# Optimization experiments

Hardware: AMD Instinct MI355X
Metric: run time of the kernel (lower is better)

## Reference

```python
import jax, jax.numpy as jnp
import numpy as np

N = 100000
E = 1600000
IN = 128
H = 256
K = 7          # n_hops + 1
INTERVAL = 3
R = K - INTERVAL + 1  # n_relations + 1 = 5


def setup_inputs() -> dict:
    key = jax.random.key(0)
    ks = jax.random.split(key, 8)
    features = jax.random.normal(ks[0], (N, IN), dtype=jnp.float32)
    W1 = jax.random.normal(ks[1], (K, IN, H), dtype=jnp.float32) * (1.0 / np.sqrt(IN))
    b1 = jnp.zeros((K, H), dtype=jnp.float32)
    W2 = jax.random.normal(ks[2], (K, H, H), dtype=jnp.float32) * (1.0 / np.sqrt(H))
    b2 = jnp.zeros((K, H), dtype=jnp.float32)
    Wr = jax.random.normal(ks[3], (R, H * INTERVAL, H), dtype=jnp.float32) * (1.0 / np.sqrt(H * INTERVAL))
    br = jnp.zeros((R, H), dtype=jnp.float32)
    row = jax.random.randint(ks[4], (E,), 0, N, dtype=jnp.int64)
    col = jax.random.randint(ks[5], (E,), 0, N, dtype=jnp.int64)
    return {"features": features, "W1": W1, "b1": b1, "W2": W2, "b2": b2,
            "Wr": Wr, "br": br, "row": row, "col": col}


def _norm_adj(row, col):
    # set_diag=True: add self loops; symm_norm: D^-1/2 (A+I) D^-1/2
    diag = jnp.arange(N, dtype=row.dtype)
    r = jnp.concatenate([row, diag])
    c = jnp.concatenate([col, diag])
    deg = jax.ops.segment_sum(jnp.ones_like(r, dtype=jnp.float32), r, num_segments=N)
    dinv = jnp.where(deg > 0, jax.lax.rsqrt(deg), 0.0)
    w = dinv[r] * dinv[c]  # [E+N]
    return r, c, w


def _forward(features, W1, b1, W2, b2, Wr, br, row, col):
    r, c, w = _norm_adj(row, col)

    def spmm(x):  # x: [N, F] -> A_hat @ x
        return jax.ops.segment_sum(x[c] * w[:, None], r, num_segments=N)

    def step(x, _):
        nx = spmm(x)
        return nx, nx

    _, hops = jax.lax.scan(step, features, None, length=K - 1)  # [K-1, N, IN]
    hop_feats = jnp.concatenate([features[None], hops], axis=0)  # [K, N, IN]

    # per-hop DeepSets (2-layer MLP with ReLU): [K, N, H]
    h = jax.nn.relu(jnp.einsum('kni,kih->knh', hop_feats, W1) + b1[:, None, :])
    h = jnp.einsum('knh,khg->kng', h, W2) + b2[:, None, :]

    hops_feats = jnp.transpose(h, (1, 0, 2))  # [N, K, H]
    # sliding windows of INTERVAL hops: [R, N, INTERVAL*H]
    wins = jnp.stack([hops_feats[:, i:i + INTERVAL, :].reshape(N, INTERVAL * H)
                      for i in range(R)], axis=0)
    rel = jax.nn.relu(jnp.einsum('rnd,rdh->rnh', wins, Wr) + br[:, None, :])  # [R, N, H]
    out = jnp.transpose(rel, (1, 0, 2)).reshape(N, R * H)  # concat over relations
    return out


def reference(features, W1, b1, W2, b2, Wr, br, row, col):
    return _forward(features, W1, b1, W2, b2, Wr, br, row, col)
```

## Files before the change

kernel.cpp:

```cpp
#include <hip/hip_runtime.h>

#define N_NODES 100000
#define E_EDGES 1600000
#define IN_F 128
#define H_F 256
#define K_HOPS 7
#define R_REL 5
#define OUT_W (R_REL * H_F)
#define SCAN_B ((N_NODES + 1023) / 1024)

typedef __attribute__((ext_vector_type(8))) short short8;
typedef __attribute__((ext_vector_type(4))) float f32x4;

#define GLOAD16(g, l) __builtin_amdgcn_global_load_lds( \
    (const __attribute__((address_space(1))) void*)(g), \
    (__attribute__((address_space(3))) void*)(l), 16, 0, 0)


__global__ void zero_int(int* __restrict__ p, int n) {
    int t = blockIdx.x * blockDim.x + threadIdx.x;
    if (t < n) p[t] = 0;
}

__global__ void deg_count(const int* __restrict__ row, int* __restrict__ deg) {
    int e = blockIdx.x * blockDim.x + threadIdx.x;
    if (e < E_EDGES) atomicAdd(&deg[row[e]], 1);
}

__global__ void dinv_compute(const int* __restrict__ deg, float* __restrict__ dinv) {
    int i = blockIdx.x * blockDim.x + threadIdx.x;
    if (i < N_NODES) dinv[i] = rsqrtf((float)(deg[i] + 1));
}

__global__ __launch_bounds__(1024) void scan1(const int* __restrict__ deg,
                                              int* __restrict__ rp, int* __restrict__ bsum) {
    __shared__ int ws[16];
    const int t = threadIdx.x, lane = t & 63, wv = t >> 6;
    int i = blockIdx.x * 1024 + t;
    int v = (i < N_NODES) ? deg[i] : 0;
    int x = v;
#pragma unroll
    for (int off = 1; off < 64; off <<= 1) {
        int n = __shfl_up(x, off, 64);
        if (lane >= off) x += n;
    }
    if (lane == 63) ws[wv] = x;
    __syncthreads();
    if (wv == 0 && lane < 16) {
        int s = ws[lane];
#pragma unroll
        for (int off = 1; off < 16; off <<= 1) {
            int n = __shfl_up(s, off, 64);
            if (lane >= off) s += n;
        }
        ws[lane] = s;
    }
    __syncthreads();
    int wbase = (wv == 0) ? 0 : ws[wv - 1];
    if (i < N_NODES) rp[i] = wbase + x - v;
    if (t == 1023) bsum[blockIdx.x] = ws[15];
}

__global__ __launch_bounds__(128) void scan2(int* __restrict__ bsum) {
    __shared__ int wtot[2];
    const int t = threadIdx.x, lane = t & 63, wv = t >> 6;
    int v = (t < SCAN_B) ? bsum[t] : 0;
    int x = v;
#pragma unroll
    for (int off = 1; off < 64; off <<= 1) {
        int n = __shfl_up(x, off, 64);
        if (lane >= off) x += n;
    }
    if (lane == 63) wtot[wv] = x;
    __syncthreads();
    int base = (wv == 1) ? wtot[0] : 0;
    if (t < SCAN_B) bsum[t] = base + x - v;
    if (t == 127) bsum[SCAN_B] = wtot[0] + wtot[1];
}

__global__ __launch_bounds__(1024) void scan3(int* __restrict__ rp,
                                              const int* __restrict__ bsum) {
    int i = blockIdx.x * 1024 + threadIdx.x;
    if (i < N_NODES) rp[i] += bsum[blockIdx.x];
    if (i == 0) rp[N_NODES] = bsum[SCAN_B];
}

__global__ void csr_scatter(const int* __restrict__ row, const int* __restrict__ col,
                            const float* __restrict__ dinv, const int* __restrict__ rowptr,
                            int* __restrict__ cursor, int* __restrict__ cols2,
                            float* __restrict__ ew) {
    int e = blockIdx.x * blockDim.x + threadIdx.x;
    if (e >= E_EDGES) return;
    int r = row[e], c = col[e];
    int pos = rowptr[r] + atomicAdd(&cursor[r], 1);
    cols2[pos] = c;
    ew[pos] = dinv[r] * dinv[c];
}

__global__ __launch_bounds__(256) void spmm_csr(
    const float4* __restrict__ x, const int* __restrict__ rowptr,
    const int* __restrict__ cols, const float* __restrict__ w,
    const float* __restrict__ dinv, float4* __restrict__ y) {
    const int wave = threadIdx.x >> 6, lane = threadIdx.x & 63;
    const int i = blockIdx.x * 4 + wave;
    if (i >= N_NODES) return;
    const int fh = lane & 31;
    const int slot = lane >> 5;
    const int jb = rowptr[i];
    const int cnt = rowptr[i + 1] - jb;

    float4 acc = make_float4(0.f, 0.f, 0.f, 0.f);
    int t = slot;
    for (; t + 6 < cnt; t += 8) {
        int c0 = cols[jb + t],     c1 = cols[jb + t + 2];
        int c2 = cols[jb + t + 4], c3 = cols[jb + t + 6];
        float ww0 = w[jb + t],     ww1 = w[jb + t + 2];
        float ww2 = w[jb + t + 4], ww3 = w[jb + t + 6];
        float4 v0 = x[(size_t)c0 * 32 + fh];
        float4 v1 = x[(size_t)c1 * 32 + fh];
        float4 v2 = x[(size_t)c2 * 32 + fh];
        float4 v3 = x[(size_t)c3 * 32 + fh];
        acc.x += ww0 * v0.x + ww1 * v1.x + ww2 * v2.x + ww3 * v3.x;
        acc.y += ww0 * v0.y + ww1 * v1.y + ww2 * v2.y + ww3 * v3.y;
        acc.z += ww0 * v0.z + ww1 * v1.z + ww2 * v2.z + ww3 * v3.z;
        acc.w += ww0 * v0.w + ww1 * v1.w + ww2 * v2.w + ww3 * v3.w;
    }
    for (; t < cnt; t += 2) {
        int c0 = cols[jb + t];
        float ww0 = w[jb + t];
        float4 v0 = x[(size_t)c0 * 32 + fh];
        acc.x += ww0 * v0.x;
        acc.y += ww0 * v0.y;
        acc.z += ww0 * v0.z;
        acc.w += ww0 * v0.w;
    }
    acc.x += __shfl_xor(acc.x, 32);
    acc.y += __shfl_xor(acc.y, 32);
    acc.z += __shfl_xor(acc.z, 32);
    acc.w += __shfl_xor(acc.w, 32);
    if (slot == 0) {
        float d = dinv[i];
        float s = d * d;
        float4 xv = x[(size_t)i * 32 + fh];
        acc.x += s * xv.x;
        acc.y += s * xv.y;
        acc.z += s * xv.z;
        acc.w += s * xv.w;
        y[(size_t)i * 32 + fh] = acc;
    }
}


__device__ __forceinline__ void f2bf_split(float v, short& h, short& l) {
    unsigned u = __float_as_uint(v);
    unsigned hb = (u + 0x7FFFu + ((u >> 16) & 1u)) >> 16;
    float fh = __uint_as_float(hb << 16);
    float r = v - fh;
    unsigned u2 = __float_as_uint(r);
    unsigned lb = (u2 + 0x7FFFu + ((u2 >> 16) & 1u)) >> 16;
    h = (short)(unsigned short)hb;
    l = (short)(unsigned short)lb;
}

__global__ __launch_bounds__(256) void wc_compute(const float* __restrict__ W2,
                                                  const float* __restrict__ Wr,
                                                  float* __restrict__ Wc) {
    __shared__ float as[8][256];
    const int z = blockIdx.x, j0 = blockIdx.y * 8, g = threadIdx.x;
    const int r = z / 3, d = z % 3, hop = r + d;
    const float* a = W2 + (size_t)hop * H_F * H_F + (size_t)j0 * H_F;
    for (int t = threadIdx.x; t < 8 * 256; t += 256)
        as[t >> 8][t & 255] = a[t];
    __syncthreads();
    const float* b = Wr + ((size_t)r * 768 + (size_t)d * H_F) * H_F + g;
    float acc[8] = {0.f, 0.f, 0.f, 0.f, 0.f, 0.f, 0.f, 0.f};
    for (int h = 0; h < H_F; ++h) {
        float bv = b[(size_t)h * H_F];
#pragma unroll
        for (int jj = 0; jj < 8; ++jj) acc[jj] += as[jj][h] * bv;
    }
#pragma unroll
    for (int jj = 0; jj < 8; ++jj)
        Wc[(size_t)z * H_F * H_F + (size_t)(j0 + jj) * H_F + g] = acc[jj];
}

__global__ __launch_bounds__(256) void bc_compute(const float* __restrict__ b2,
                                                  const float* __restrict__ Wr,
                                                  const float* __restrict__ br,
                                                  float* __restrict__ bc) {
    const int r = blockIdx.x, g = threadIdx.x;
    float acc = br[(size_t)r * H_F + g];
    for (int t = 0; t < 3 * H_F; ++t) {
        float bv = b2[(size_t)(r + t / H_F) * H_F + (t % H_F)];
        acc += bv * Wr[((size_t)r * 768 + t) * H_F + g];
    }
    bc[(size_t)r * H_F + g] = acc;
}

__global__ void transpose_convert(const float* __restrict__ in, short* __restrict__ oh,
                                  short* __restrict__ ol, int Kd, int grp) {
    __shared__ float t[32][33];
    const int i0 = blockIdx.x * 32, n0 = blockIdx.y * 32, z = blockIdx.z;
    const int tx = threadIdx.x, ty = threadIdx.y;
    const int outLd = grp * Kd;
    const float* ip = in + (size_t)z * Kd * 256;
#pragma unroll
    for (int j = 0; j < 4; ++j)
        t[ty + 8 * j][tx] = ip[(size_t)(i0 + ty + 8 * j) * 256 + n0 + tx];
    __syncthreads();
    size_t base = (size_t)(z / grp) * 256 * outLd + (size_t)(z % grp) * Kd;
#pragma unroll
    for (int j = 0; j < 4; ++j) {
        float v = t[tx][ty + 8 * j];
        short hb, lb;
        f2bf_split(v, hb, lb);
        size_t o = base + (size_t)(n0 + ty + 8 * j) * outLd + i0 + tx;
        oh[o] = hb;
        ol[o] = lb;
    }
}


#define LROW 40

__global__ __launch_bounds__(256, 2) void gemm_mlp(
    const float* __restrict__ A,
    const short* __restrict__ BTh, const short* __restrict__ BTl,
    short* __restrict__ Ch, short* __restrict__ Cl,
    const float* __restrict__ bias, int M)
{
    __shared__ short lds_buf[4 * 128 * LROW];
    short* Ah = lds_buf;
    short* Al = lds_buf + 128 * LROW;
    short* Bh = lds_buf + 2 * 128 * LROW;
    short* Bl = lds_buf + 3 * 128 * LROW;

    const int tid = threadIdx.x;
    const int lane = tid & 63, wave = tid >> 6;
    const int wm = wave & 1, wn = wave >> 1;
    const int fr = lane & 15, fg = lane >> 4;
    const int m0 = blockIdx.y * 128;
    const int n0 = blockIdx.x * 128;

    const int sr = tid >> 1;
    const int sc = (tid & 1) * 16;
    const bool avalid = (m0 + sr) < M;
    const int arow = avalid ? (m0 + sr) : (M - 1);

    f32x4 ga[4];
    short8 gbh[2], gbl[2];
    {
        const float* ap = A + (size_t)arow * IN_F + sc;
        const short* bph = BTh + (size_t)(n0 + sr) * IN_F + sc;
        const short* bpl = BTl + (size_t)(n0 + sr) * IN_F + sc;
#pragma unroll
        for (int l = 0; l < 4; ++l) ga[l] = *(const f32x4*)(ap + 4 * l);
        gbh[0] = *(const short8*)bph;  gbh[1] = *(const short8*)(bph + 8);
        gbl[0] = *(const short8*)bpl;  gbl[1] = *(const short8*)(bpl + 8);
    }

    f32x4 acc[4][4];
#pragma unroll
    for (int i = 0; i < 4; ++i)
#pragma unroll
        for (int j = 0; j < 4; ++j) acc[i][j] = (f32x4)0.f;

    const int nk = IN_F / 32;
    for (int kk = 0; kk < nk; ++kk) {
        __syncthreads();
        {
            short8 vh[2], vl[2];
#pragma unroll
            for (int l = 0; l < 4; ++l) {
                f32x4 v = ga[l];
                if (!avalid) v = (f32x4)0.f;
#pragma unroll
                for (int e = 0; e < 4; ++e) {
                    short hb, lb;
                    f2bf_split(v[e], hb, lb);
                    vh[l >> 1][(l & 1) * 4 + e] = hb;
                    vl[l >> 1][(l & 1) * 4 + e] = lb;
                }
            }
            *(short8*)(Ah + sr * LROW + sc)     = vh[0];
            *(short8*)(Ah + sr * LROW + sc + 8) = vh[1];
            *(short8*)(Al + sr * LROW + sc)     = vl[0];
            *(short8*)(Al + sr * LROW + sc + 8) = vl[1];
            *(short8*)(Bh + sr * LROW + sc)     = gbh[0];
            *(short8*)(Bh + sr * LROW + sc + 8) = gbh[1];
            *(short8*)(Bl + sr * LROW + sc)     = gbl[0];
            *(short8*)(Bl + sr * LROW + sc + 8) = gbl[1];
        }
        __syncthreads();

        if (kk + 1 < nk) {
            int k0 = (kk + 1) * 32;
            const float* ap = A + (size_t)arow * IN_F + k0 + sc;
            const short* bph = BTh + (size_t)(n0 + sr) * IN_F + k0 + sc;
            const short* bpl = BTl + (size_t)(n0 + sr) * IN_F + k0 + sc;
#pragma unroll
            for (int l = 0; l < 4; ++l) ga[l] = *(const f32x4*)(ap + 4 * l);
            gbh[0] = *(const short8*)(bph);  gbh[1] = *(const short8*)(bph + 8);
            gbl[0] = *(const short8*)(bpl);  gbl[1] = *(const short8*)(bpl + 8);
        }

        short8 afh[4], afl[4], bfh[4], bfl[4];
#pragma unroll
        for (int mf = 0; mf < 4; ++mf) {
            int r = wm * 64 + mf * 16 + fr;
            afh[mf] = *(const short8*)(Ah + r * LROW + fg * 8);
            afl[mf] = *(const short8*)(Al + r * LROW + fg * 8);
        }
#pragma unroll
        for (int nf = 0; nf < 4; ++nf) {
            int r = wn * 64 + nf * 16 + fr;
            bfh[nf] = *(const short8*)(Bh + r * LROW + fg * 8);
            bfl[nf] = *(const short8*)(Bl + r * LROW + fg * 8);
        }
#pragma unroll
        for (int mf = 0; mf < 4; ++mf)
#pragma unroll
            for (int nf = 0; nf < 4; ++nf) {
                acc[mf][nf] = __builtin_amdgcn_mfma_f32_16x16x32_bf16(
                    afh[mf], bfh[nf], acc[mf][nf], 0, 0, 0);
                acc[mf][nf] = __builtin_amdgcn_mfma_f32_16x16x32_bf16(
                    afh[mf], bfl[nf], acc[mf][nf], 0, 0, 0);
                acc[mf][nf] = __builtin_amdgcn_mfma_f32_16x16x32_bf16(
                    afl[mf], bfh[nf], acc[mf][nf], 0, 0, 0);
            }
    }

#pragma unroll
    for (int nf = 0; nf < 4; ++nf) {
        int colg = n0 + wn * 64 + nf * 16 + fr;
        float bv = bias[colg];
#pragma unroll
        for (int mf = 0; mf < 4; ++mf) {
            int rowbase = m0 + wm * 64 + mf * 16 + fg * 4;
#pragma unroll
            for (int j = 0; j < 4; ++j) {
                int rowg = rowbase + j;
                if (rowg < M) {
                    float v = fmaxf(acc[mf][nf][j] + bv, 0.f);
                    short hb, lb;
                    f2bf_split(v, hb, lb);
                    size_t idx = (size_t)rowg * H_F + colg;
                    Ch[idx] = hb;
                    Cl[idx] = lb;
                }
            }
        }
    }
}


__global__ __launch_bounds__(512, 2) void gemm_rel(
    const short* __restrict__ h1h, const short* __restrict__ h1l, long hopStride,
    const short* __restrict__ wch, const short* __restrict__ wcl,
    float* __restrict__ outB, const float* __restrict__ bcB, int M, int nwg)
{
    __shared__ short lds[2][4][8192];

    const int bid = blockIdx.x;
    const int q8 = nwg >> 3, r8 = nwg & 7;
    const int xcd = bid & 7, idx = bid >> 3;
    const int wgid = (xcd < r8) ? (xcd * (q8 + 1) + idx)
                                : (r8 * (q8 + 1) + (xcd - r8) * q8 + idx);
    const int rrel = wgid % R_REL;
    const int mblk = wgid / R_REL;
    const int m0 = mblk * 256;

    const int tid = threadIdx.x;
    const int lane = tid & 63, wave = tid >> 6;
    const int wm = wave & 1, wn = wave >> 1;
    const int fr = lane & 15, fg = lane >> 4;

    const short* Agh = h1h + (size_t)rrel * hopStride;
    const short* Agl = h1l + (size_t)rrel * hopStride;
    const short* BTh = wch + (size_t)rrel * 256 * 768;
    const short* BTl = wcl + (size_t)rrel * 256 * 768;
    float* C = outB + (size_t)rrel * H_F;
    const float* bias = bcB + (size_t)rrel * H_F;

    const int kstart = ((3 - (rrel % 3)) % 3) * 8;

    int aoff[2], boff[2], loff[2];
#pragma unroll
    for (int p = 0; p < 2; ++p) {
        int c = wave * 2 + p;
        int r = c * 16 + (lane >> 2);
        int u = lane & 3;
        int g = (u - (r >> 1)) & 3;
        int ar = m0 + r; if (ar >= M) ar = M - 1;
        aoff[p] = ar * H_F + g * 8;
        boff[p] = r * 768 + g * 8;
        loff[p] = c * 512;
    }

#define STAGE_REL(buf, kg) do {                                                  \
        int hop_ = (kg) >> 8, kin_ = (kg) & 255;                                 \
        const short* ah_ = Agh + (size_t)hop_ * hopStride + kin_;                \
        const short* al_ = Agl + (size_t)hop_ * hopStride + kin_;                \
        const short* bh_ = BTh + (kg);                                           \
        const short* bl_ = BTl + (kg);                                           \
        GLOAD16(ah_ + aoff[0], &lds[buf][0][loff[0]]);                           \
        GLOAD16(ah_ + aoff[1], &lds[buf][0][loff[1]]);                           \
        GLOAD16(al_ + aoff[0], &lds[buf][1][loff[0]]);                           \
        GLOAD16(al_ + aoff[1], &lds[buf][1][loff[1]]);                           \
        GLOAD16(bh_ + boff[0], &lds[buf][2][loff[0]]);                           \
        GLOAD16(bh_ + boff[1], &lds[buf][2][loff[1]]);                           \
        GLOAD16(bl_ + boff[0], &lds[buf][3][loff[0]]);                           \
        GLOAD16(bl_ + boff[1], &lds[buf][3][loff[1]]);                           \
    } while (0)

#define KIDX(t) ((((t) + kstart) % nk) * 32)

    f32x4 acc[8][4];
#pragma unroll
    for (int i = 0; i < 8; ++i)
#pragma unroll
        for (int j = 0; j < 4; ++j) acc[i][j] = (f32x4)0.f;

    const int nk = 768 / 32;

    STAGE_REL(0, KIDX(0));
    STAGE_REL(1, KIDX(1));

    int cur = 0;
    for (int kt = 0; kt < nk; ++kt) {
        if (kt + 1 < nk) {
            asm volatile("s_waitcnt vmcnt(8)" ::: "memory");
        } else {
            asm volatile("s_waitcnt vmcnt(0)" ::: "memory");
        }
        __builtin_amdgcn_sched_barrier(0);
        __builtin_amdgcn_s_barrier();
        __builtin_amdgcn_sched_barrier(0);

        const short* Ahc = &lds[cur][0][0];
        const short* Alc = &lds[cur][1][0];
        const short* Bhc = &lds[cur][2][0];
        const short* Blc = &lds[cur][3][0];

        short8 bfh[4], bfl[4];
#pragma unroll
        for (int nf = 0; nf < 4; ++nf) {
            int rb = wn * 64 + nf * 16 + fr;
            int ub = (fg + (rb >> 1)) & 3;
            bfh[nf] = *(const short8*)(Bhc + rb * 32 + ub * 8);
            bfl[nf] = *(const short8*)(Blc + rb * 32 + ub * 8);
        }
        __builtin_amdgcn_s_setprio(1);
#pragma unroll
        for (int mf = 0; mf < 8; ++mf) {
            int ra = wm * 128 + mf * 16 + fr;
            int ua = (fg + (ra >> 1)) & 3;
            short8 ah = *(const short8*)(Ahc + ra * 32 + ua * 8);
            short8 al = *(const short8*)(Alc + ra * 32 + ua * 8);
#pragma unroll
            for (int nf = 0; nf < 4; ++nf) {
                acc[mf][nf] = __builtin_amdgcn_mfma_f32_16x16x32_bf16(
                    ah, bfh[nf], acc[mf][nf], 0, 0, 0);
                acc[mf][nf] = __builtin_amdgcn_mfma_f32_16x16x32_bf16(
                    ah, bfl[nf], acc[mf][nf], 0, 0, 0);
                acc[mf][nf] = __builtin_amdgcn_mfma_f32_16x16x32_bf16(
                    al, bfh[nf], acc[mf][nf], 0, 0, 0);
            }
        }
        __builtin_amdgcn_s_setprio(0);

        __builtin_amdgcn_sched_barrier(0);
        __builtin_amdgcn_s_barrier();
        __builtin_amdgcn_sched_barrier(0);

        if (kt + 2 < nk) STAGE_REL(cur, KIDX(kt + 2));
        cur ^= 1;
    }

#pragma unroll
    for (int nf = 0; nf < 4; ++nf) {
        int colg = wn * 64 + nf * 16 + fr;
        float bv = bias[colg];
#pragma unroll
        for (int mf = 0; mf < 8; ++mf) {
            int rowbase = m0 + wm * 128 + mf * 16 + fg * 4;
#pragma unroll
            for (int j = 0; j < 4; ++j) {
                int rowg = rowbase + j;
                if (rowg < M)
                    C[(size_t)rowg * OUT_W + colg] = fmaxf(acc[mf][nf][j] + bv, 0.f);
            }
        }
    }
#undef STAGE_REL
#undef KIDX
}


template <int MODE>
__global__ __launch_bounds__(256, 2) void gemm_presplit(
    const short* __restrict__ Agh, const short* __restrict__ Agl, int lda,
    const short* __restrict__ BTh, const short* __restrict__ BTl, int ldb, int Kd,
    float* __restrict__ C, int ldc, const float* __restrict__ bias, int M)
{
    __shared__ short lds_buf[4 * 128 * LROW];
    short* Ah = lds_buf;
    short* Al = lds_buf + 128 * LROW;
    short* Bh = lds_buf + 2 * 128 * LROW;
    short* Bl = lds_buf + 3 * 128 * LROW;

    const int tid = threadIdx.x;
    const int lane = tid & 63, wave = tid >> 6;
    const int wm = wave & 1, wn = wave >> 1;
    const int fr = lane & 15, fg = lane >> 4;
    const int m0 = blockIdx.y * 128;
    const int n0 = blockIdx.x * 128;

    const int sr = tid >> 1;
    const int sc = (tid & 1) * 16;
    const bool avalid = (m0 + sr) < M;
    const int arow = avalid ? (m0 + sr) : (M - 1);

    short8 gah[2], gal[2], gbh[2], gbl[2];
    {
        const short* aph = Agh + (size_t)arow * lda + sc;
        const short* apl = Agl + (size_t)arow * lda + sc;
        const short* bph = BTh + (size_t)(n0 + sr) * ldb + sc;
        const short* bpl = BTl + (size_t)(n0 + sr) * ldb + sc;
        gah[0] = *(const short8*)aph;  gah[1] = *(const short8*)(aph + 8);
        gal[0] = *(const short8*)apl;  gal[1] = *(const short8*)(apl + 8);
        gbh[0] = *(const short8*)bph;  gbh[1] = *(const short8*)(bph + 8);
        gbl[0] = *(const short8*)bpl;  gbl[1] = *(const short8*)(bpl + 8);
    }

    f32x4 acc[4][4];
#pragma unroll
    for (int i = 0; i < 4; ++i)
#pragma unroll
        for (int j = 0; j < 4; ++j) acc[i][j] = (f32x4)0.f;

    const int nk = Kd / 32;
    for (int kk = 0; kk < nk; ++kk) {
        __syncthreads();
        *(short8*)(Ah + sr * LROW + sc)     = gah[0];
        *(short8*)(Ah + sr * LROW + sc + 8) = gah[1];
        *(short8*)(Al + sr * LROW + sc)     = gal[0];
        *(short8*)(Al + sr * LROW + sc + 8) = gal[1];
        *(short8*)(Bh + sr * LROW + sc)     = gbh[0];
        *(short8*)(Bh + sr * LROW + sc + 8) = gbh[1];
        *(short8*)(Bl + sr * LROW + sc)     = gbl[0];
        *(short8*)(Bl + sr * LROW + sc + 8) = gbl[1];
        __syncthreads();

        if (kk + 1 < nk) {
            int k0 = (kk + 1) * 32;
            const short* aph = Agh + (size_t)arow * lda + k0 + sc;
            const short* apl = Agl + (size_t)arow * lda + k0 + sc;
            const short* bph = BTh + (size_t)(n0 + sr) * ldb + k0 + sc;
            const short* bpl = BTl + (size_t)(n0 + sr) * ldb + k0 + sc;
            gah[0] = *(const short8*)aph;  gah[1] = *(const short8*)(aph + 8);
            gal[0] = *(const short8*)apl;  gal[1] = *(const short8*)(apl + 8);
            gbh[0] = *(const short8*)bph;  gbh[1] = *(const short8*)(bph + 8);
            gbl[0] = *(const short8*)bpl;  gbl[1] = *(const short8*)(bpl + 8);
        }

        short8 afh[4], afl[4], bfh[4], bfl[4];
#pragma unroll
        for (int mf = 0; mf < 4; ++mf) {
            int r = wm * 64 + mf * 16 + fr;
            afh[mf] = *(const short8*)(Ah + r * LROW + fg * 8);
            afl[mf] = *(const short8*)(Al + r * LROW + fg * 8);
        }
#pragma unroll
        for (int nf = 0; nf < 4; ++nf) {
            int r = wn * 64 + nf * 16 + fr;
            bfh[nf] = *(const short8*)(Bh + r * LROW + fg * 8);
            bfl[nf] = *(const short8*)(Bl + r * LROW + fg * 8);
        }
#pragma unroll
        for (int mf = 0; mf < 4; ++mf)
#pragma unroll
            for (int nf = 0; nf < 4; ++nf) {
                acc[mf][nf] = __builtin_amdgcn_mfma_f32_16x16x32_bf16(
                    afh[mf], bfh[nf], acc[mf][nf], 0, 0, 0);
                acc[mf][nf] = __builtin_amdgcn_mfma_f32_16x16x32_bf16(
                    afh[mf], bfl[nf], acc[mf][nf], 0, 0, 0);
                acc[mf][nf] = __builtin_amdgcn_mfma_f32_16x16x32_bf16(
                    afl[mf], bfh[nf], acc[mf][nf], 0, 0, 0);
            }
    }

#pragma unroll
    for (int nf = 0; nf < 4; ++nf) {
        int colg = n0 + wn * 64 + nf * 16 + fr;
        float bv = (MODE == 0) ? bias[colg] : 0.f;
#pragma unroll
        for (int mf = 0; mf < 4; ++mf) {
            int rowbase = m0 + wm * 64 + mf * 16 + fg * 4;
#pragma unroll
            for (int j = 0; j < 4; ++j) {
                int rowg = rowbase + j;
                if (rowg < M) {
                    size_t idx = (size_t)rowg * ldc + colg;
                    float v = acc[mf][nf][j] + bv;
                    if (MODE >= 2) v += C[idx];
                    if (MODE & 1) v = fmaxf(v, 0.f);
                    C[idx] = v;
                }
            }
        }
    }
}


extern "C" void kernel_launch(void* const* d_in, const int* in_sizes, int n_in,
                              void* d_out, int out_size, void* d_ws, size_t ws_size,
                              hipStream_t stream) {
    const float* features = (const float*)d_in[0];
    const float* W1 = (const float*)d_in[1];
    const float* b1 = (const float*)d_in[2];
    const float* W2 = (const float*)d_in[3];
    const float* b2 = (const float*)d_in[4];
    const float* Wr = (const float*)d_in[5];
    const float* br = (const float*)d_in[6];
    const int* row = (const int*)d_in[7];
    const int* col = (const int*)d_in[8];
    float* out = (float*)d_out;

    char* ws = (char*)d_ws;
    int* deg = (int*)ws;
    int* rowptr = (int*)(ws + (1ull << 20));
    float* dinv = (float*)(ws + (2ull << 20));
    int* bsum = (int*)(ws + (3ull << 20));
    int* cols2 = (int*)(ws + (4ull << 20));
    float* ew = (float*)(ws + (11ull << 20));
    short* w1h = (short*)(ws + (18ull << 20));
    short* w1l = (short*)(ws + (19ull << 20));
    float* wc32 = (float*)(ws + (20ull << 20));
    short* wch = (short*)(ws + (24ull << 20));
    short* wcl = (short*)(ws + (26ull << 20));
    float* bc = (float*)(ws + (28ull << 20));
    float* xa = (float*)(ws + (32ull << 20));
    float* xb = (float*)(ws + (96ull << 20));
    short* h1h = (short*)(ws + (160ull << 20));
    short* h1l = (short*)(ws + (576ull << 20));

    const bool windowed = ws_size >= (1000ull << 20);

    zero_int<<<(N_NODES + 255) / 256, 256, 0, stream>>>(deg, N_NODES);
    deg_count<<<(E_EDGES + 255) / 256, 256, 0, stream>>>(row, deg);
    dinv_compute<<<(N_NODES + 255) / 256, 256, 0, stream>>>(deg, dinv);
    scan1<<<SCAN_B, 1024, 0, stream>>>(deg, rowptr, bsum);
    scan2<<<1, 128, 0, stream>>>(bsum);
    scan3<<<SCAN_B, 1024, 0, stream>>>(rowptr, bsum);
    zero_int<<<(N_NODES + 255) / 256, 256, 0, stream>>>(deg, N_NODES);
    csr_scatter<<<(E_EDGES + 255) / 256, 256, 0, stream>>>(row, col, dinv, rowptr,
                                                           deg, cols2, ew);

    wc_compute<<<dim3(15, 32), 256, 0, stream>>>(W2, Wr, wc32);
    bc_compute<<<R_REL, 256, 0, stream>>>(b2, Wr, br, bc);

    dim3 tb(32, 8);
    transpose_convert<<<dim3(IN_F / 32, 8, K_HOPS), tb, 0, stream>>>(W1, w1h, w1l, IN_F, 1);
    transpose_convert<<<dim3(H_F / 32, 8, 15), tb, 0, stream>>>(wc32, wch, wcl, H_F, 3);

    const float* xcur = features;
    float* bufs[2] = {xa, xb};
    for (int k = 0; k < K_HOPS; ++k) {
        short* h1hd = windowed ? (h1h + (size_t)k * N_NODES * H_F) : h1h;
        short* h1ld = windowed ? (h1l + (size_t)k * N_NODES * H_F) : h1l;
        dim3 grid(2, (N_NODES + 127) / 128);
        gemm_mlp<<<grid, 256, 0, stream>>>(xcur, w1h + (size_t)k * 256 * IN_F,
                                           w1l + (size_t)k * 256 * IN_F,
                                           h1hd, h1ld, b1 + (size_t)k * H_F, N_NODES);

        if (!windowed) {
            int rlo = (k - 2 < 0) ? 0 : (k - 2);
            int rhi = (k < R_REL - 1) ? k : (R_REL - 1);
            for (int r = rlo; r <= rhi; ++r) {
                int d = k - r;
                const short* Bh = wch + (size_t)r * 256 * 768 + (size_t)d * H_F;
                const short* Bl = wcl + (size_t)r * 256 * 768 + (size_t)d * H_F;
                float* Cp = out + (size_t)r * H_F;
                if (k == r)
                    gemm_presplit<0><<<grid, 256, 0, stream>>>(
                        h1h, h1l, H_F, Bh, Bl, 768, H_F, Cp, OUT_W,
                        bc + (size_t)r * H_F, N_NODES);
                else if (k == r + 2)
                    gemm_presplit<3><<<grid, 256, 0, stream>>>(
                        h1h, h1l, H_F, Bh, Bl, 768, H_F, Cp, OUT_W, nullptr, N_NODES);
                else
                    gemm_presplit<2><<<grid, 256, 0, stream>>>(
                        h1h, h1l, H_F, Bh, Bl, 768, H_F, Cp, OUT_W, nullptr, N_NODES);
            }
        }

        if (k < K_HOPS - 1) {
            float* xn = bufs[k & 1];
            spmm_csr<<<(N_NODES + 3) / 4, 256, 0, stream>>>(
                (const float4*)xcur, rowptr, cols2, ew, dinv, (float4*)xn);
            xcur = xn;
        }
    }

    if (windowed) {
        int mblocks = (N_NODES + 255) / 256;
        int nwg = mblocks * R_REL;
        gemm_rel<<<nwg, 512, 0, stream>>>(h1h, h1l, (long)N_NODES * H_F,
                                          wch, wcl, out, bc, N_NODES, nwg);
    }
}
```

Before: 2.173 ms.

## Fuse per-hop MLP GEMM and SpMM into one interleaved launch

Adds a combined kernel in which one of every sixteen blocks runs the first-layer MLP GEMM tile for the current hop and the remaining blocks run SpMM rows that produce the next hop's features. Both parts read the same input features and have no dependency on each other, so the compute-bound GEMM and the memory-bound gather can overlap on the GPU. This also removes one launch per hop in the windowed path. In exchange, both workloads share one launch-bounds setting and one shared-memory allocation, which can limit occupancy for the SpMM blocks, and correctness depends on the block-index mapping being right.

```diff
diff --git a/kernel.cpp b/kernel.cpp
--- a/kernel.cpp
+++ b/kernel.cpp
@@ -97,13 +97,216 @@
     ew[pos] = dinv[r] * dinv[c];
 }
 
-__global__ __launch_bounds__(256) void spmm_csr(
+
+__device__ __forceinline__ void f2bf_split(float v, short& h, short& l) {
+    unsigned u = __float_as_uint(v);
+    unsigned hb = (u + 0x7FFFu + ((u >> 16) & 1u)) >> 16;
+    float fh = __uint_as_float(hb << 16);
+    float r = v - fh;
+    unsigned u2 = __float_as_uint(r);
+    unsigned lb = (u2 + 0x7FFFu + ((u2 >> 16) & 1u)) >> 16;
+    h = (short)(unsigned short)hb;
+    l = (short)(unsigned short)lb;
+}
+
+__global__ __launch_bounds__(256) void wc_compute(const float* __restrict__ W2,
+                                                  const float* __restrict__ Wr,
+                                                  float* __restrict__ Wc) {
+    __shared__ float as[8][256];
+    const int z = blockIdx.x, j0 = blockIdx.y * 8, g = threadIdx.x;
+    const int r = z / 3, d = z % 3, hop = r + d;
+    const float* a = W2 + (size_t)hop * H_F * H_F + (size_t)j0 * H_F;
+    for (int t = threadIdx.x; t < 8 * 256; t += 256)
+        as[t >> 8][t & 255] = a[t];
+    __syncthreads();
+    const float* b = Wr + ((size_t)r * 768 + (size_t)d * H_F) * H_F + g;
+    float acc[8] = {0.f, 0.f, 0.f, 0.f, 0.f, 0.f, 0.f, 0.f};
+    for (int h = 0; h < H_F; ++h) {
+        float bv = b[(size_t)h * H_F];
+#pragma unroll
+        for (int jj = 0; jj < 8; ++jj) acc[jj] += as[jj][h] * bv;
+    }
+#pragma unroll
+    for (int jj = 0; jj < 8; ++jj)
+        Wc[(size_t)z * H_F * H_F + (size_t)(j0 + jj) * H_F + g] = acc[jj];
+}
+
+__global__ __launch_bounds__(256) void bc_compute(const float* __restrict__ b2,
+                                                  const float* __restrict__ Wr,
+                                                  const float* __restrict__ br,
+                                                  float* __restrict__ bc) {
+    const int r = blockIdx.x, g = threadIdx.x;
+    float acc = br[(size_t)r * H_F + g];
+    for (int t = 0; t < 3 * H_F; ++t) {
+        float bv = b2[(size_t)(r + t / H_F) * H_F + (t % H_F)];
+        acc += bv * Wr[((size_t)r * 768 + t) * H_F + g];
+    }
+    bc[(size_t)r * H_F + g] = acc;
+}
+
+__global__ void transpose_convert(const float* __restrict__ in, short* __restrict__ oh,
+                                  short* __restrict__ ol, int Kd, int grp) {
+    __shared__ float t[32][33];
+    const int i0 = blockIdx.x * 32, n0 = blockIdx.y * 32, z = blockIdx.z;
+    const int tx = threadIdx.x, ty = threadIdx.y;
+    const int outLd = grp * Kd;
+    const float* ip = in + (size_t)z * Kd * 256;
+#pragma unroll
+    for (int j = 0; j < 4; ++j)
+        t[ty + 8 * j][tx] = ip[(size_t)(i0 + ty + 8 * j) * 256 + n0 + tx];
+    __syncthreads();
+    size_t base = (size_t)(z / grp) * 256 * outLd + (size_t)(z % grp) * Kd;
+#pragma unroll
+    for (int j = 0; j < 4; ++j) {
+        float v = t[tx][ty + 8 * j];
+        short hb, lb;
+        f2bf_split(v, hb, lb);
+        size_t o = base + (size_t)(n0 + ty + 8 * j) * outLd + i0 + tx;
+        oh[o] = hb;
+        ol[o] = lb;
+    }
+}
+
+
+#define LROW 40
+
+__device__ __forceinline__ void mlp1_body(
+    short* lds_buf, int midx,
+    const float* __restrict__ A,
+    const short* __restrict__ BTh, const short* __restrict__ BTl,
+    short* __restrict__ Ch, short* __restrict__ Cl,
+    const float* __restrict__ bias, int M)
+{
+    short* Ah = lds_buf;
+    short* Al = lds_buf + 128 * LROW;
+    short* Bh = lds_buf + 2 * 128 * LROW;
+    short* Bl = lds_buf + 3 * 128 * LROW;
+
+    const int tid = threadIdx.x;
+    const int lane = tid & 63, wave = tid >> 6;
+    const int wm = wave & 1, wn = wave >> 1;
+    const int fr = lane & 15, fg = lane >> 4;
+    const int m0 = (midx >> 1) * 128;
+    const int n0 = (midx & 1) * 128;
+
+    const int sr = tid >> 1;
+    const int sc = (tid & 1) * 16;
+    const bool avalid = (m0 + sr) < M;
+    const int arow = avalid ? (m0 + sr) : (M - 1);
+
+    f32x4 ga[4];
+    short8 gbh[2], gbl[2];
+    {
+        const float* ap = A + (size_t)arow * IN_F + sc;
+        const short* bph = BTh + (size_t)(n0 + sr) * IN_F + sc;
+        const short* bpl = BTl + (size_t)(n0 + sr) * IN_F + sc;
+#pragma unroll
+        for (int l = 0; l < 4; ++l) ga[l] = *(const f32x4*)(ap + 4 * l);
+        gbh[0] = *(const short8*)bph;  gbh[1] = *(const short8*)(bph + 8);
+        gbl[0] = *(const short8*)bpl;  gbl[1] = *(const short8*)(bpl + 8);
+    }
+
+    f32x4 acc[4][4];
+#pragma unroll
+    for (int i = 0; i < 4; ++i)
+#pragma unroll
+        for (int j = 0; j < 4; ++j) acc[i][j] = (f32x4)0.f;
+
+    const int nk = IN_F / 32;
+    for (int kk = 0; kk < nk; ++kk) {
+        __syncthreads();
+        {
+            short8 vh[2], vl[2];
+#pragma unroll
+            for (int l = 0; l < 4; ++l) {
+                f32x4 v = ga[l];
+                if (!avalid) v = (f32x4)0.f;
+#pragma unroll
+                for (int e = 0; e < 4; ++e) {
+                    short hb, lb;
+                    f2bf_split(v[e], hb, lb);
+                    vh[l >> 1][(l & 1) * 4 + e] = hb;
+                    vl[l >> 1][(l & 1) * 4 + e] = lb;
+                }
+            }
+            *(short8*)(Ah + sr * LROW + sc)     = vh[0];
+            *(short8*)(Ah + sr * LROW + sc + 8) = vh[1];
+            *(short8*)(Al + sr * LROW + sc)     = vl[0];
+            *(short8*)(Al + sr * LROW + sc + 8) = vl[1];
+            *(short8*)(Bh + sr * LROW + sc)     = gbh[0];
+            *(short8*)(Bh + sr * LROW + sc + 8) = gbh[1];
+            *(short8*)(Bl + sr * LROW + sc)     = gbl[0];
+            *(short8*)(Bl + sr * LROW + sc + 8) = gbl[1];
+        }
+        __syncthreads();
+
+        if (kk + 1 < nk) {
+            int k0 = (kk + 1) * 32;
+            const float* ap = A + (size_t)arow * IN_F + k0 + sc;
+            const short* bph = BTh + (size_t)(n0 + sr) * IN_F + k0 + sc;
+            const short* bpl = BTl + (size_t)(n0 + sr) * IN_F + k0 + sc;
+#pragma unroll
+            for (int l = 0; l < 4; ++l) ga[l] = *(const f32x4*)(ap + 4 * l);
+            gbh[0] = *(const short8*)(bph);  gbh[1] = *(const short8*)(bph + 8);
+            gbl[0] = *(const short8*)(bpl);  gbl[1] = *(const short8*)(bpl + 8);
+        }
+
+        short8 afh[4], afl[4], bfh[4], bfl[4];
+#pragma unroll
+        for (int mf = 0; mf < 4; ++mf) {
+            int r = wm * 64 + mf * 16 + fr;
+            afh[mf] = *(const short8*)(Ah + r * LROW + fg * 8);
+            afl[mf] = *(const short8*)(Al + r * LROW + fg * 8);
+        }
+#pragma unroll
+        for (int nf = 0; nf < 4; ++nf) {
+            int r = wn * 64 + nf * 16 + fr;
+            bfh[nf] = *(const short8*)(Bh + r * LROW + fg * 8);
+            bfl[nf] = *(const short8*)(Bl + r * LROW + fg * 8);
+        }
+#pragma unroll
+        for (int mf = 0; mf < 4; ++mf)
+#pragma unroll
+            for (int nf = 0; nf < 4; ++nf) {
+                acc[mf][nf] = __builtin_amdgcn_mfma_f32_16x16x32_bf16(
+                    afh[mf], bfh[nf], acc[mf][nf], 0, 0, 0);
+                acc[mf][nf] = __builtin_amdgcn_mfma_f32_16x16x32_bf16(
+                    afh[mf], bfl[nf], acc[mf][nf], 0, 0, 0);
+                acc[mf][nf] = __builtin_amdgcn_mfma_f32_16x16x32_bf16(
+                    afl[mf], bfh[nf], acc[mf][nf], 0, 0, 0);
+            }
+    }
+
+#pragma unroll
+    for (int nf = 0; nf < 4; ++nf) {
+        int colg = n0 + wn * 64 + nf * 16 + fr;
+        float bv = bias[colg];
+#pragma unroll
+        for (int mf = 0; mf < 4; ++mf) {
+            int rowbase = m0 + wm * 64 + mf * 16 + fg * 4;
+#pragma unroll
+            for (int j = 0; j < 4; ++j) {
+                int rowg = rowbase + j;
+                if (rowg < M) {
+                    float v = fmaxf(acc[mf][nf][j] + bv, 0.f);
+                    short hb, lb;
+                    f2bf_split(v, hb, lb);
+                    size_t idx = (size_t)rowg * H_F + colg;
+                    Ch[idx] = hb;
+                    Cl[idx] = lb;
+                }
+            }
+        }
+    }
+}
+
+__device__ __forceinline__ void spmm_body(
+    int i,
     const float4* __restrict__ x, const int* __restrict__ rowptr,
     const int* __restrict__ cols, const float* __restrict__ w,
-    const float* __restrict__ dinv, float4* __restrict__ y) {
-    const int wave = threadIdx.x >> 6, lane = threadIdx.x & 63;
-    const int i = blockIdx.x * 4 + wave;
-    if (i >= N_NODES) return;
+    const float* __restrict__ dinv, float4* __restrict__ y)
+{
+    const int lane = threadIdx.x & 63;
     const int fh = lane & 31;
     const int slot = lane >> 5;
     const int jb = rowptr[i];
@@ -151,78 +354,6 @@
 }
 
 
-__device__ __forceinline__ void f2bf_split(float v, short& h, short& l) {
-    unsigned u = __float_as_uint(v);
-    unsigned hb = (u + 0x7FFFu + ((u >> 16) & 1u)) >> 16;
-    float fh = __uint_as_float(hb << 16);
-    float r = v - fh;
-    unsigned u2 = __float_as_uint(r);
-    unsigned lb = (u2 + 0x7FFFu + ((u2 >> 16) & 1u)) >> 16;
-    h = (short)(unsigned short)hb;
-    l = (short)(unsigned short)lb;
-}
-
-__global__ __launch_bounds__(256) void wc_compute(const float* __restrict__ W2,
-                                                  const float* __restrict__ Wr,
-                                                  float* __restrict__ Wc) {
-    __shared__ float as[8][256];
-    const int z = blockIdx.x, j0 = blockIdx.y * 8, g = threadIdx.x;
-    const int r = z / 3, d = z % 3, hop = r + d;
-    const float* a = W2 + (size_t)hop * H_F * H_F + (size_t)j0 * H_F;
-    for (int t = threadIdx.x; t < 8 * 256; t += 256)
-        as[t >> 8][t & 255] = a[t];
-    __syncthreads();
-    const float* b = Wr + ((size_t)r * 768 + (size_t)d * H_F) * H_F + g;
-    float acc[8] = {0.f, 0.f, 0.f, 0.f, 0.f, 0.f, 0.f, 0.f};
-    for (int h = 0; h < H_F; ++h) {
-        float bv = b[(size_t)h * H_F];
-#pragma unroll
-        for (int jj = 0; jj < 8; ++jj) acc[jj] += as[jj][h] * bv;
-    }
-#pragma unroll
-    for (int jj = 0; jj < 8; ++jj)
-        Wc[(size_t)z * H_F * H_F + (size_t)(j0 + jj) * H_F + g] = acc[jj];
-}
-
-__global__ __launch_bounds__(256) void bc_compute(const float* __restrict__ b2,
-                                                  const float* __restrict__ Wr,
-                                                  const float* __restrict__ br,
-                                                  float* __restrict__ bc) {
-    const int r = blockIdx.x, g = threadIdx.x;
-    float acc = br[(size_t)r * H_F + g];
-    for (int t = 0; t < 3 * H_F; ++t) {
-        float bv = b2[(size_t)(r + t / H_F) * H_F + (t % H_F)];
-        acc += bv * Wr[((size_t)r * 768 + t) * H_F + g];
-    }
-    bc[(size_t)r * H_F + g] = acc;
-}
-
-__global__ void transpose_convert(const float* __restrict__ in, short* __restrict__ oh,
-                                  short* __restrict__ ol, int Kd, int grp) {
-    __shared__ float t[32][33];
-    const int i0 = blockIdx.x * 32, n0 = blockIdx.y * 32, z = blockIdx.z;
-    const int tx = threadIdx.x, ty = threadIdx.y;
-    const int outLd = grp * Kd;
-    const float* ip = in + (size_t)z * Kd * 256;
-#pragma unroll
-    for (int j = 0; j < 4; ++j)
-        t[ty + 8 * j][tx] = ip[(size_t)(i0 + ty + 8 * j) * 256 + n0 + tx];
-    __syncthreads();
-    size_t base = (size_t)(z / grp) * 256 * outLd + (size_t)(z % grp) * Kd;
-#pragma unroll
-    for (int j = 0; j < 4; ++j) {
-        float v = t[tx][ty + 8 * j];
-        short hb, lb;
-        f2bf_split(v, hb, lb);
-        size_t o = base + (size_t)(n0 + ty + 8 * j) * outLd + i0 + tx;
-        oh[o] = hb;
-        ol[o] = lb;
-    }
-}
-
-
-#define LROW 40
-
 __global__ __launch_bounds__(256, 2) void gemm_mlp(
     const float* __restrict__ A,
     const short* __restrict__ BTh, const short* __restrict__ BTl,
@@ -230,126 +361,37 @@
     const float* __restrict__ bias, int M)
 {
     __shared__ short lds_buf[4 * 128 * LROW];
-    short* Ah = lds_buf;
-    short* Al = lds_buf + 128 * LROW;
-    short* Bh = lds_buf + 2 * 128 * LROW;
-    short* Bl = lds_buf + 3 * 128 * LROW;
-
-    const int tid = threadIdx.x;
-    const int lane = tid & 63, wave = tid >> 6;
-    const int wm = wave & 1, wn = wave >> 1;
-    const int fr = lane & 15, fg = lane >> 4;
-    const int m0 = blockIdx.y * 128;
-    const int n0 = blockIdx.x * 128;
-
-    const int sr = tid >> 1;
-    const int sc = (tid & 1) * 16;
-    const bool avalid = (m0 + sr) < M;
-    const int arow = avalid ? (m0 + sr) : (M - 1);
-
-    f32x4 ga[4];
-    short8 gbh[2], gbl[2];
-    {
-        const float* ap = A + (size_t)arow * IN_F + sc;
-        const short* bph = BTh + (size_t)(n0 + sr) * IN_F + sc;
-        const short* bpl = BTl + (size_t)(n0 + sr) * IN_F + sc;
-#pragma unroll
-        for (int l = 0; l < 4; ++l) ga[l] = *(const f32x4*)(ap + 4 * l);
-        gbh[0] = *(const short8*)bph;  gbh[1] = *(const short8*)(bph + 8);
-        gbl[0] = *(const short8*)bpl;  gbl[1] = *(const short8*)(bpl + 8);
-    }
-
-    f32x4 acc[4][4];
-#pragma unroll
-    for (int i = 0; i < 4; ++i)
-#pragma unroll
-        for (int j = 0; j < 4; ++j) acc[i][j] = (f32x4)0.f;
-
-    const int nk = IN_F / 32;
-    for (int kk = 0; kk < nk; ++kk) {
-        __syncthreads();
-        {
-            short8 vh[2], vl[2];
-#pragma unroll
-            for (int l = 0; l < 4; ++l) {
-                f32x4 v = ga[l];
-                if (!avalid) v = (f32x4)0.f;
-#pragma unroll
-                for (int e = 0; e < 4; ++e) {
-                    short hb, lb;
-                    f2bf_split(v[e], hb, lb);
-                    vh[l >> 1][(l & 1) * 4 + e] = hb;
-                    vl[l >> 1][(l & 1) * 4 + e] = lb;
-                }
-            }
-            *(short8*)(Ah + sr * LROW + sc)     = vh[0];
-            *(short8*)(Ah + sr * LROW + sc + 8) = vh[1];
-            *(short8*)(Al + sr * LROW + sc)     = vl[0];
-            *(short8*)(Al + sr * LROW + sc + 8) = vl[1];
-            *(short8*)(Bh + sr * LROW + sc)     = gbh[0];
-            *(short8*)(Bh + sr * LROW + sc + 8) = gbh[1];
-            *(short8*)(Bl + sr * LROW + sc)     = gbl[0];
-            *(short8*)(Bl + sr * LROW + sc + 8) = gbl[1];
-        }
-        __syncthreads();
-
-        if (kk + 1 < nk) {
-            int k0 = (kk + 1) * 32;
-            const float* ap = A + (size_t)arow * IN_F + k0 + sc;
-            const short* bph = BTh + (size_t)(n0 + sr) * IN_F + k0 + sc;
-            const short* bpl = BTl + (size_t)(n0 + sr) * IN_F + k0 + sc;
-#pragma unroll
-            for (int l = 0; l < 4; ++l) ga[l] = *(const f32x4*)(ap + 4 * l);
-            gbh[0] = *(const short8*)(bph);  gbh[1] = *(const short8*)(bph + 8);
-            gbl[0] = *(const short8*)(bpl);  gbl[1] = *(const short8*)(bpl + 8);
-        }
-
-        short8 afh[4], afl[4], bfh[4], bfl[4];
-#pragma unroll
-        for (int mf = 0; mf < 4; ++mf) {
-            int r = wm * 64 + mf * 16 + fr;
-            afh[mf] = *(const short8*)(Ah + r * LROW + fg * 8);
-            afl[mf] = *(const short8*)(Al + r * LROW + fg * 8);
-        }
-#pragma unroll
-        for (int nf = 0; nf < 4; ++nf) {
-            int r = wn * 64 + nf * 16 + fr;
-            bfh[nf] = *(const short8*)(Bh + r * LROW + fg * 8);
-            bfl[nf] = *(const short8*)(Bl + r * LROW + fg * 8);
-        }
-#pragma unroll
-        for (int mf = 0; mf < 4; ++mf)
-#pragma unroll
-            for (int nf = 0; nf < 4; ++nf) {
-                acc[mf][nf] = __builtin_amdgcn_mfma_f32_16x16x32_bf16(
-                    afh[mf], bfh[nf], acc[mf][nf], 0, 0, 0);
-                acc[mf][nf] = __builtin_amdgcn_mfma_f32_16x16x32_bf16(
-                    afh[mf], bfl[nf], acc[mf][nf], 0, 0, 0);
-                acc[mf][nf] = __builtin_amdgcn_mfma_f32_16x16x32_bf16(
-                    afl[mf], bfh[nf], acc[mf][nf], 0, 0, 0);
-            }
-    }
-
-#pragma unroll
-    for (int nf = 0; nf < 4; ++nf) {
-        int colg = n0 + wn * 64 + nf * 16 + fr;
-        float bv = bias[colg];
-#pragma unroll
-        for (int mf = 0; mf < 4; ++mf) {
-            int rowbase = m0 + wm * 64 + mf * 16 + fg * 4;
-#pragma unroll
-            for (int j = 0; j < 4; ++j) {
-                int rowg = rowbase + j;
-                if (rowg < M) {
-                    float v = fmaxf(acc[mf][nf][j] + bv, 0.f);
-                    short hb, lb;
-                    f2bf_split(v, hb, lb);
-                    size_t idx = (size_t)rowg * H_F + colg;
-                    Ch[idx] = hb;
-                    Cl[idx] = lb;
-                }
-            }
-        }
+    mlp1_body(lds_buf, blockIdx.x, A, BTh, BTl, Ch, Cl, bias, M);
+}
+
+__global__ __launch_bounds__(256) void spmm_csr(
+    const float4* __restrict__ x, const int* __restrict__ rowptr,
+    const int* __restrict__ cols, const float* __restrict__ w,
+    const float* __restrict__ dinv, float4* __restrict__ y) {
+    const int i = blockIdx.x * 4 + (threadIdx.x >> 6);
+    if (i < N_NODES) spmm_body(i, x, rowptr, cols, w, dinv, y);
+}
+
+
+__global__ __launch_bounds__(256, 4) void mlp_spmm(
+    const float* __restrict__ xcur,
+    const short* __restrict__ BTh, const short* __restrict__ BTl,
+    short* __restrict__ Ch, short* __restrict__ Cl,
+    const float* __restrict__ bias,
+    const int* __restrict__ rowptr, const int* __restrict__ cols,
+    const float* __restrict__ w, const float* __restrict__ dinv,
+    float4* __restrict__ y, int nm)
+{
+    __shared__ short lds_buf[4 * 128 * LROW];
+    const int bid = blockIdx.x;
+    const int thresh = nm * 16;
+    if (bid < thresh && (bid & 15) == 0) {
+        mlp1_body(lds_buf, bid >> 4, xcur, BTh, BTl, Ch, Cl, bias, N_NODES);
+    } else {
+        int sidx = (bid < thresh) ? (bid - (bid >> 4) - 1) : (bid - nm);
+        int i = sidx * 4 + (threadIdx.x >> 6);
+        if (i < N_NODES)
+            spmm_body(i, (const float4*)xcur, rowptr, cols, w, dinv, y);
     }
 }
 
@@ -666,40 +708,51 @@
 
     const float* xcur = features;
     float* bufs[2] = {xa, xb};
+    const int nm = 2 * ((N_NODES + 127) / 128);
+    const int ns = (N_NODES + 3) / 4;
     for (int k = 0; k < K_HOPS; ++k) {
         short* h1hd = windowed ? (h1h + (size_t)k * N_NODES * H_F) : h1h;
         short* h1ld = windowed ? (h1l + (size_t)k * N_NODES * H_F) : h1l;
-        dim3 grid(2, (N_NODES + 127) / 128);
-        gemm_mlp<<<grid, 256, 0, stream>>>(xcur, w1h + (size_t)k * 256 * IN_F,
-                                           w1l + (size_t)k * 256 * IN_F,
-                                           h1hd, h1ld, b1 + (size_t)k * H_F, N_NODES);
-
-        if (!windowed) {
-            int rlo = (k - 2 < 0) ? 0 : (k - 2);
-            int rhi = (k < R_REL - 1) ? k : (R_REL - 1);
-            for (int r = rlo; r <= rhi; ++r) {
-                int d = k - r;
-                const short* Bh = wch + (size_t)r * 256 * 768 + (size_t)d * H_F;
-                const short* Bl = wcl + (size_t)r * 256 * 768 + (size_t)d * H_F;
-                float* Cp = out + (size_t)r * H_F;
-                if (k == r)
-                    gemm_presplit<0><<<grid, 256, 0, stream>>>(
-                        h1h, h1l, H_F, Bh, Bl, 768, H_F, Cp, OUT_W,
-                        bc + (size_t)r * H_F, N_NODES);
-                else if (k == r + 2)
-                    gemm_presplit<3><<<grid, 256, 0, stream>>>(
-                        h1h, h1l, H_F, Bh, Bl, 768, H_F, Cp, OUT_W, nullptr, N_NODES);
-                else
-                    gemm_presplit<2><<<grid, 256, 0, stream>>>(
-                        h1h, h1l, H_F, Bh, Bl, 768, H_F, Cp, OUT_W, nullptr, N_NODES);
+
+        if (windowed && k < K_HOPS - 1) {
+            float* xn = bufs[k & 1];
+            mlp_spmm<<<nm + ns, 256, 0, stream>>>(
+                xcur, w1h + (size_t)k * 256 * IN_F, w1l + (size_t)k * 256 * IN_F,
+                h1hd, h1ld, b1 + (size_t)k * H_F,
+                rowptr, cols2, ew, dinv, (float4*)xn, nm);
+            xcur = xn;
+        } else {
+            dim3 grid(2, (N_NODES + 127) / 128);
+            gemm_mlp<<<dim3(nm), 256, 0, stream>>>(
+                xcur, w1h + (size_t)k * 256 * IN_F, w1l + (size_t)k * 256 * IN_F,
+                h1hd, h1ld, b1 + (size_t)k * H_F, N_NODES);
+
+            if (!windowed) {
+                int rlo = (k - 2 < 0) ? 0 : (k - 2);
+                int rhi = (k < R_REL - 1) ? k : (R_REL - 1);
+                for (int r = rlo; r <= rhi; ++r) {
+                    int d = k - r;
+                    const short* Bh = wch + (size_t)r * 256 * 768 + (size_t)d * H_F;
+                    const short* Bl = wcl + (size_t)r * 256 * 768 + (size_t)d * H_F;
+                    float* Cp = out + (size_t)r * H_F;
+                    if (k == r)
+                        gemm_presplit<0><<<grid, 256, 0, stream>>>(
+                            h1h, h1l, H_F, Bh, Bl, 768, H_F, Cp, OUT_W,
+                            bc + (size_t)r * H_F, N_NODES);
+                    else if (k == r + 2)
+                        gemm_presplit<3><<<grid, 256, 0, stream>>>(
+                            h1h, h1l, H_F, Bh, Bl, 768, H_F, Cp, OUT_W, nullptr, N_NODES);
+                    else
+                        gemm_presplit<2><<<grid, 256, 0, stream>>>(
+                            h1h, h1l, H_F, Bh, Bl, 768, H_F, Cp, OUT_W, nullptr, N_NODES);
+                }
+                if (k < K_HOPS - 1) {
+                    float* xn = bufs[k & 1];
+                    spmm_csr<<<ns, 256, 0, stream>>>(
+                        (const float4*)xcur, rowptr, cols2, ew, dinv, (float4*)xn);
+                    xcur = xn;
+                }
             }
-        }
-
-        if (k < K_HOPS - 1) {
-            float* xn = bufs[k & 1];
-            spmm_csr<<<(N_NODES + 3) / 4, 256, 0, stream>>>(
-                (const float4*)xcur, rowptr, cols2, ew, dinv, (float4*)xn);
-            xcur = xn;
         }
     }
 
```

Result: slower. 4.589 ms (+111.2%).

## Interleave next-tile global-to-LDS prefetch with MFMA phases in relation GEMM

Applied to the files above, without the earlier changes.

The relation GEMM's k-loop is split into four MFMA phases, each covering two row fragments. The next k-tile's global_load_lds copies are spread across the phase boundaries, so each LDS chunk is refilled as soon as every wave has consumed it, instead of issuing all prefetches after the full compute block. The goal is to overlap memory traffic with MFMA work and hide the load latency. In exchange there are four barrier pairs per iteration instead of one, plus an lgkmcnt(0) wait in every phase, which adds synchronisation overhead.

```diff
diff --git a/kernel.cpp b/kernel.cpp
--- a/kernel.cpp
+++ b/kernel.cpp
@@ -354,6 +354,44 @@
 }
 
 
+__device__ __forceinline__ f32x4 mfma16(short8 a, short8 b, f32x4 c) {
+    return __builtin_amdgcn_mfma_f32_16x16x32_bf16(a, b, c, 0, 0, 0);
+}
+
+template <int MFA, int MFB>
+__device__ __forceinline__ void rel_phase(
+    const short* Ahc, const short* Alc,
+    const short8* bfh, const short8* bfl,
+    f32x4 (&acc)[8][4], int wm, int fr, int fg)
+{
+    const int ra0 = wm * 128 + MFA * 16 + fr;
+    const int ua0 = (fg + (ra0 >> 1)) & 3;
+    short8 ahA = *(const short8*)(Ahc + ra0 * 32 + ua0 * 8);
+    short8 alA = *(const short8*)(Alc + ra0 * 32 + ua0 * 8);
+    const int ra1 = wm * 128 + MFB * 16 + fr;
+    const int ua1 = (fg + (ra1 >> 1)) & 3;
+    short8 ahB = *(const short8*)(Ahc + ra1 * 32 + ua1 * 8);
+    short8 alB = *(const short8*)(Alc + ra1 * 32 + ua1 * 8);
+    __builtin_amdgcn_sched_barrier(0);
+    __builtin_amdgcn_s_barrier();
+    asm volatile("s_waitcnt lgkmcnt(0)" ::: "memory");
+    __builtin_amdgcn_sched_barrier(0);
+    __builtin_amdgcn_s_setprio(1);
+#pragma unroll
+    for (int nf = 0; nf < 4; ++nf) {
+        acc[MFA][nf] = mfma16(ahA, bfh[nf], acc[MFA][nf]);
+        acc[MFA][nf] = mfma16(ahA, bfl[nf], acc[MFA][nf]);
+        acc[MFA][nf] = mfma16(alA, bfh[nf], acc[MFA][nf]);
+        acc[MFB][nf] = mfma16(ahB, bfh[nf], acc[MFB][nf]);
+        acc[MFB][nf] = mfma16(ahB, bfl[nf], acc[MFB][nf]);
+        acc[MFB][nf] = mfma16(alB, bfh[nf], acc[MFB][nf]);
+    }
+    __builtin_amdgcn_s_setprio(0);
+    __builtin_amdgcn_sched_barrier(0);
+    __builtin_amdgcn_s_barrier();
+    __builtin_amdgcn_sched_barrier(0);
+}
+
 __global__ __launch_bounds__(512, 2) void gemm_rel(
     const short* __restrict__ h1h, const short* __restrict__ h1l, long hopStride,
     const short* __restrict__ wch, const short* __restrict__ wcl,
@@ -397,22 +435,29 @@
         loff[p] = c * 512;
     }
 
-#define STAGE_REL(buf, kg) do {                                                  \
-        int hop_ = (kg) >> 8, kin_ = (kg) & 255;                                 \
-        const short* ah_ = Agh + (size_t)hop_ * hopStride + kin_;                \
-        const short* al_ = Agl + (size_t)hop_ * hopStride + kin_;                \
-        const short* bh_ = BTh + (kg);                                           \
-        const short* bl_ = BTl + (kg);                                           \
-        GLOAD16(ah_ + aoff[0], &lds[buf][0][loff[0]]);                           \
-        GLOAD16(ah_ + aoff[1], &lds[buf][0][loff[1]]);                           \
-        GLOAD16(al_ + aoff[0], &lds[buf][1][loff[0]]);                           \
-        GLOAD16(al_ + aoff[1], &lds[buf][1][loff[1]]);                           \
-        GLOAD16(bh_ + boff[0], &lds[buf][2][loff[0]]);                           \
-        GLOAD16(bh_ + boff[1], &lds[buf][2][loff[1]]);                           \
-        GLOAD16(bl_ + boff[0], &lds[buf][3][loff[0]]);                           \
-        GLOAD16(bl_ + boff[1], &lds[buf][3][loff[1]]);                           \
+#define STAGE_B4(buf, kg) do {                                                  \
+        const short* bh_ = BTh + (kg);                                          \
+        const short* bl_ = BTl + (kg);                                          \
+        GLOAD16(bh_ + boff[0], &lds[buf][2][loff[0]]);                          \
+        GLOAD16(bh_ + boff[1], &lds[buf][2][loff[1]]);                          \
+        GLOAD16(bl_ + boff[0], &lds[buf][3][loff[0]]);                          \
+        GLOAD16(bl_ + boff[1], &lds[buf][3][loff[1]]);                          \
     } while (0)
 
+#define STAGE_A(buf, kg, p) do {                                                \
+        int hop_ = (kg) >> 8, kin_ = (kg) & 255;                                \
+        const short* ah_ = Agh + (size_t)hop_ * hopStride + kin_;               \
+        const short* al_ = Agl + (size_t)hop_ * hopStride + kin_;               \
+        GLOAD16(ah_ + aoff[p], &lds[buf][0][loff[p]]);                          \
+        GLOAD16(al_ + aoff[p], &lds[buf][1][loff[p]]);                          \
+    } while (0)
+
+#define STAGE_FULL(buf, kg) do {                                                \
+        STAGE_A(buf, kg, 0);                                                    \
+        STAGE_A(buf, kg, 1);                                                    \
+        STAGE_B4(buf, kg);                                                      \
+    } while (0)
+
 #define KIDX(t) ((((t) + kstart) % nk) * 32)
 
     f32x4 acc[8][4];
@@ -422,12 +467,16 @@
         for (int j = 0; j < 4; ++j) acc[i][j] = (f32x4)0.f;
 
     const int nk = 768 / 32;
-
-    STAGE_REL(0, KIDX(0));
-    STAGE_REL(1, KIDX(1));
+    const bool wodd = (wave & 1) != 0;
+
+    STAGE_FULL(0, KIDX(0));
+    STAGE_FULL(1, KIDX(1));
 
     int cur = 0;
     for (int kt = 0; kt < nk; ++kt) {
+        const bool pf = (kt + 2 < nk);
+        const int kg2 = KIDX(kt + 2);
+
         if (kt + 1 < nk) {
             asm volatile("s_waitcnt vmcnt(8)" ::: "memory");
         } else {
@@ -450,30 +499,22 @@
             bfh[nf] = *(const short8*)(Bhc + rb * 32 + ub * 8);
             bfl[nf] = *(const short8*)(Blc + rb * 32 + ub * 8);
         }
-        __builtin_amdgcn_s_setprio(1);
-#pragma unroll
-        for (int mf = 0; mf < 8; ++mf) {
-            int ra = wm * 128 + mf * 16 + fr;
-            int ua = (fg + (ra >> 1)) & 3;
-            short8 ah = *(const short8*)(Ahc + ra * 32 + ua * 8);
-            short8 al = *(const short8*)(Alc + ra * 32 + ua * 8);
-#pragma unroll
-            for (int nf = 0; nf < 4; ++nf) {
-                acc[mf][nf] = __builtin_amdgcn_mfma_f32_16x16x32_bf16(
-                    ah, bfh[nf], acc[mf][nf], 0, 0, 0);
-                acc[mf][nf] = __builtin_amdgcn_mfma_f32_16x16x32_bf16(
-                    ah, bfl[nf], acc[mf][nf], 0, 0, 0);
-                acc[mf][nf] = __builtin_amdgcn_mfma_f32_16x16x32_bf16(
-                    al, bfh[nf], acc[mf][nf], 0, 0, 0);
-            }
-        }
-        __builtin_amdgcn_s_setprio(0);
-
-        __builtin_amdgcn_sched_barrier(0);
-        __builtin_amdgcn_s_barrier();
-        __builtin_amdgcn_sched_barrier(0);
-
-        if (kt + 2 < nk) STAGE_REL(cur, KIDX(kt + 2));
+        rel_phase<0, 4>(Ahc, Alc, bfh, bfl, acc, wm, fr, fg);
+
+        if (pf) {
+            STAGE_B4(cur, kg2);
+            if (!wodd) STAGE_A(cur, kg2, 0);
+        }
+        rel_phase<1, 5>(Ahc, Alc, bfh, bfl, acc, wm, fr, fg);
+
+        if (pf && !wodd) STAGE_A(cur, kg2, 1);
+        rel_phase<2, 6>(Ahc, Alc, bfh, bfl, acc, wm, fr, fg);
+
+        if (pf && wodd) STAGE_A(cur, kg2, 0);
+        rel_phase<3, 7>(Ahc, Alc, bfh, bfl, acc, wm, fr, fg);
+
+        if (pf && wodd) STAGE_A(cur, kg2, 1);
+
         cur ^= 1;
     }
 
@@ -492,7 +533,9 @@
             }
         }
     }
-#undef STAGE_REL
+#undef STAGE_B4
+#undef STAGE_A
+#undef STAGE_FULL
 #undef KIDX
 }
 
```

After: 2.148 ms. Within noise of the previous version (-1.1%).
